# Kernel tuning notes

Measured on AMD Instinct MI355X. Metric: run time of the kernel, lower is better.

Reference implementation:

```python
import jax, jax.numpy as jnp
import numpy as np

B, S, DIM = 4, 4096, 1024
BASE_COUPLING = 0.1
NUM_CYCLES = 3


def _gelu(x):
    # torch nn.GELU default = exact erf formulation
    return jax.nn.gelu(x, approximate=False)


def setup_inputs() -> dict:
    key = jax.random.key(0)
    ks = jax.random.split(key, 9)
    d = DIM

    def w(k, fan_in, fan_out):
        return (jax.random.normal(k, (fan_in, fan_out), dtype=jnp.float32)
                / np.sqrt(fan_in).astype(np.float32))

    inp = {"x": jax.random.normal(ks[0], (B, S, d), dtype=jnp.float32)}
    # coupling_net: dim -> dim -> dim/2 -> dim/4 -> 1
    cn_dims = [(d, d), (d, d // 2), (d // 2, d // 4), (d // 4, 1)]
    for i, (a, b) in enumerate(cn_dims):
        inp[f"cn_w{i+1}"] = w(ks[1 + i], a, b)
        inp[f"cn_b{i+1}"] = jnp.zeros((b,), dtype=jnp.float32)
    # global_context_net: dim -> dim/2 -> dim/4 -> 1
    gc_dims = [(d, d // 2), (d // 2, d // 4), (d // 4, 1)]
    for i, (a, b) in enumerate(gc_dims):
        inp[f"gc_w{i+1}"] = w(ks[5 + i], a, b)
        inp[f"gc_b{i+1}"] = jnp.zeros((b,), dtype=jnp.float32)
    inp["adaptive_range"] = jnp.full((1,), 0.2, dtype=jnp.float32)
    return inp


def _coupling_net(h, w1, b1, w2, b2, w3, b3, w4, b4):
    h = _gelu(h @ w1 + b1)
    h = _gelu(h @ w2 + b2)
    h = _gelu(h @ w3 + b3)
    return jax.nn.sigmoid(h @ w4 + b4)  # [..., 1]


def _global_net(h, w1, b1, w2, b2, w3, b3):
    h = _gelu(h @ w1 + b1)
    h = _gelu(h @ w2 + b2)
    return jax.nn.sigmoid(h @ w3 + b3)  # [b, 1, 1]


def _twist(x):
    # x: [b, s, dim]; omega = first half, pi = second half;
    # each split again into real/imag halves -> quarters [or, oi, pr, pim].
    # omega_new = [pr, -pim], pi_new = [-or, oi]  (position-independent elementwise swap)
    o_r, o_i, p_r, p_i = jnp.split(x, 4, axis=-1)
    return jnp.concatenate([p_r, -p_i, -o_r, o_i], axis=-1)


def reference(x, cn_w1, cn_b1, cn_w2, cn_b2, cn_w3, cn_b3, cn_w4, cn_b4,
              gc_w1, gc_b1, gc_w2, gc_b2, gc_w3, gc_b3, adaptive_range):
    global_context = x.mean(axis=1, keepdims=True)  # [b, 1, dim]
    gf = _global_net(global_context, gc_w1, gc_b1, gc_w2, gc_b2, gc_w3, gc_b3)  # [b,1,1]
    out = x
    for _ in range(NUM_CYCLES):
        tf = _coupling_net(out, cn_w1, cn_b1, cn_w2, cn_b2, cn_w3, cn_b3, cn_w4, cn_b4)  # [b,s,1]
        combined = 0.7 * gf + 0.3 * tf
        coupling = BASE_COUPLING + adaptive_range * (combined - 0.5) * 2.0  # [b,s,1]
        out = out + coupling * _twist(out)
    return out
```

## Files before the change

kernel.cpp:

```cpp
#include <hip/hip_runtime.h>
#include <hip/hip_bf16.h>

#define PB 4
#define PS 4096
#define PD 1024
#define ROWS (PB * PS)
#define NUM_CYCLES 3
#define BASE_COUPLING 0.1f
#define WSCALE 256.0f
#define INV_WSCALE (1.0f / 256.0f)

typedef __attribute__((ext_vector_type(8))) short bf16x8;
typedef __attribute__((ext_vector_type(4))) float f32x4;

__device__ __forceinline__ float geluf(float x) {
    return 0.5f * x * (1.0f + erff(x * 0.70710678118654752440f));
}
__device__ __forceinline__ float gelu_fast(float x) {
    float u = (x + 0.044715f * x * x * x) * 2.3022077f;
    return x * __builtin_amdgcn_rcpf(1.0f + exp2f(-u));
}
__device__ __forceinline__ float sigmf_(float x) {
    return 1.0f / (1.0f + expf(-x));
}
__device__ __forceinline__ uint2 pk4(float4 v) {
    __hip_bfloat16 h[4] = {__float2bfloat16(v.x), __float2bfloat16(v.y),
                           __float2bfloat16(v.z), __float2bfloat16(v.w)};
    return *reinterpret_cast<uint2*>(h);
}
__device__ __forceinline__ float4 axpy4(float4 a, float s, float4 b) {
    return make_float4(fmaf(s, b.x, a.x), fmaf(s, b.y, a.y),
                       fmaf(s, b.z, a.z), fmaf(s, b.w, a.w));
}
__device__ __forceinline__ float bf2f(unsigned short u) {
    unsigned int w = ((unsigned int)u) << 16;
    return __builtin_bit_cast(float, w);
}
__device__ __forceinline__ float4 ubf2f4(uint2 u) {
    unsigned short h[4];
    *reinterpret_cast<uint2*>(h) = u;
    return make_float4(bf2f(h[0]), bf2f(h[1]), bf2f(h[2]), bf2f(h[3]));
}
__device__ __forceinline__ unsigned char f2e4m3(float x) {
    unsigned int u = __builtin_bit_cast(unsigned int, x);
    unsigned int s = (u >> 24) & 0x80u;
    float ax = __builtin_fabsf(x);
    if (!(ax >= 0.015625f)) return (unsigned char)s;
    if (ax >= 464.0f) return (unsigned char)(s | 0x7Eu);
    unsigned int au = u & 0x7FFFFFFFu;
    unsigned int lsb = (au >> 20) & 1u;
    au += 0x0007FFFFu + lsb;
    unsigned int e = (au >> 23) - 127u + 7u;
    unsigned int m = (au >> 20) & 7u;
    if (e >= 16u) return (unsigned char)(s | 0x7Eu);
    return (unsigned char)(s | (e << 3) | m);
}
__device__ __forceinline__ unsigned int pk8(float4 v) {
    return (unsigned int)f2e4m3(v.x) | ((unsigned int)f2e4m3(v.y) << 8) |
           ((unsigned int)f2e4m3(v.z) << 16) | ((unsigned int)f2e4m3(v.w) << 24);
}

#define GLD_LDS16(gsrc, ldst)                                                        \
    __builtin_amdgcn_global_load_lds(                                                \
        (const __attribute__((address_space(1))) void*)(gsrc),                       \
        (__attribute__((address_space(3))) void*)(ldst), 16, 0, 0)

#define ASM_VMCNT4() asm volatile("s_waitcnt vmcnt(4)" ::: "memory")
#define ASM_VMCNT0() asm volatile("s_waitcnt vmcnt(0)" ::: "memory")
#define ASM_LGKM0()  asm volatile("s_waitcnt lgkmcnt(0)" ::: "memory")
#define SCHED_FENCE() __builtin_amdgcn_sched_barrier(0)

__global__ __launch_bounds__(256) void copy_mean_cvt_kernel(const float* __restrict__ x,
                                                            unsigned char* __restrict__ outb8,
                                                            float* __restrict__ part) {
    int b = blockIdx.x >> 7, sc = blockIdx.x & 127;
    size_t base = ((size_t)b * PS + (size_t)sc * 32) * PD;
    const float4* x4 = reinterpret_cast<const float4*>(x + base);
    unsigned int* o8 = reinterpret_cast<unsigned int*>(outb8 + base);
    int t = threadIdx.x;
    float4 acc = make_float4(0.f, 0.f, 0.f, 0.f);
    for (int r = 0; r < 32; ++r) {
        float4 v = x4[r * 256 + t];
        o8[r * 256 + t] = pk8(v);
        acc.x += v.x; acc.y += v.y; acc.z += v.z; acc.w += v.w;
    }
    reinterpret_cast<float4*>(part + ((size_t)(b * 128 + sc)) * PD)[t] = acc;
}

__global__ __launch_bounds__(256) void mean_stage2(const float* __restrict__ part,
                                                   float* __restrict__ gc) {
    int b = blockIdx.x, t = threadIdx.x;
    float4 s = make_float4(0.f, 0.f, 0.f, 0.f);
    for (int c = 0; c < 128; ++c) {
        float4 v = reinterpret_cast<const float4*>(part + ((size_t)(b * 128 + c)) * PD)[t];
        s.x += v.x; s.y += v.y; s.z += v.z; s.w += v.w;
    }
    s.x *= (1.0f / 4096.0f); s.y *= (1.0f / 4096.0f);
    s.z *= (1.0f / 4096.0f); s.w *= (1.0f / 4096.0f);
    reinterpret_cast<float4*>(gc + (size_t)b * PD)[t] = s;
}

__global__ __launch_bounds__(256) void transpose_w_kernel(const float* __restrict__ W,
                                                          __hip_bfloat16* __restrict__ Wt,
                                                          int K, int N) {
    __shared__ float t[32][33];
    int k0 = blockIdx.x * 32, n0 = blockIdx.y * 32;
    int tx = threadIdx.x & 31, ty = threadIdx.x >> 5;
#pragma unroll
    for (int i = 0; i < 32; i += 8)
        t[ty + i][tx] = W[(size_t)(k0 + ty + i) * N + n0 + tx];
    __syncthreads();
#pragma unroll
    for (int i = 0; i < 32; i += 8)
        Wt[(size_t)(n0 + ty + i) * K + k0 + tx] = __float2bfloat16(t[tx][ty + i]);
}

__global__ __launch_bounds__(256) void transpose_w8_kernel(const float* __restrict__ W,
                                                           unsigned char* __restrict__ Wt8,
                                                           int K, int N) {
    __shared__ float t[32][33];
    int k0 = blockIdx.x * 32, n0 = blockIdx.y * 32;
    int tx = threadIdx.x & 31, ty = threadIdx.x >> 5;
#pragma unroll
    for (int i = 0; i < 32; i += 8)
        t[ty + i][tx] = W[(size_t)(k0 + ty + i) * N + n0 + tx];
    __syncthreads();
#pragma unroll
    for (int i = 0; i < 32; i += 8)
        Wt8[(size_t)(n0 + ty + i) * K + k0 + tx] = f2e4m3(t[tx][ty + i] * WSCALE);
}

__global__ __launch_bounds__(256) void gn1_kernel(const float* __restrict__ gc,
                                                  const float* __restrict__ w1,
                                                  const float* __restrict__ b1,
                                                  float* __restrict__ g1) {
    __shared__ float gcs[1024];
    __shared__ float red[4][64];
    int b = blockIdx.x, j0 = blockIdx.y * 64;
    int t = threadIdx.x, wave = t >> 6, lane = t & 63;
    for (int i = t; i < 1024; i += 256) gcs[i] = gc[(size_t)b * PD + i];
    __syncthreads();
    int j = j0 + lane;
    float a = 0.f;
    int k0 = wave * 256;
    for (int k = k0; k < k0 + 256; ++k) a += gcs[k] * w1[(size_t)k * 512 + j];
    red[wave][lane] = a;
    __syncthreads();
    if (wave == 0) {
        float v = red[0][lane] + red[1][lane] + red[2][lane] + red[3][lane] + b1[j];
        g1[(size_t)b * 512 + j] = geluf(v);
    }
}

__global__ __launch_bounds__(256) void gn2_kernel(const float* __restrict__ g1,
                                                  const float* __restrict__ w2,
                                                  const float* __restrict__ b2,
                                                  float* __restrict__ g2) {
    __shared__ float g1s[512];
    __shared__ float red[4][64];
    int b = blockIdx.x, j0 = blockIdx.y * 64;
    int t = threadIdx.x, wave = t >> 6, lane = t & 63;
    for (int i = t; i < 512; i += 256) g1s[i] = g1[(size_t)b * 512 + i];
    __syncthreads();
    int j = j0 + lane;
    float a = 0.f;
    int k0 = wave * 128;
    for (int k = k0; k < k0 + 128; ++k) a += g1s[k] * w2[(size_t)k * 256 + j];
    red[wave][lane] = a;
    __syncthreads();
    if (wave == 0) {
        float v = red[0][lane] + red[1][lane] + red[2][lane] + red[3][lane] + b2[j];
        g2[(size_t)b * 256 + j] = geluf(v);
    }
}

__global__ __launch_bounds__(256) void gn3_kernel(const float* __restrict__ g2,
                                                  const float* __restrict__ w3,
                                                  const float* __restrict__ b3,
                                                  float* __restrict__ gf) {
    __shared__ float red[256];
    int b = blockIdx.x, t = threadIdx.x;
    red[t] = g2[(size_t)b * 256 + t] * w3[t];
    __syncthreads();
    for (int s = 128; s > 0; s >>= 1) {
        if (t < s) red[t] += red[t + s];
        __syncthreads();
    }
    if (t == 0) gf[b] = sigmf_(red[0] + b3[0]);
}

template <int OUTFP8>
__global__ __launch_bounds__(256, 2) void gemm128f8_kernel(
    const unsigned char* __restrict__ A,
    const unsigned char* __restrict__ Wt,
    const float* __restrict__ bias,
    unsigned char* __restrict__ C8,
    __hip_bfloat16* __restrict__ Cb,
    int K, int N) {
    __shared__ __align__(16) unsigned char Als[2][128 * 64];
    __shared__ __align__(16) unsigned char Bls[2][128 * 64];
    const int tid = threadIdx.x;
    const int wave = tid >> 6, lane = tid & 63;
    const int m0 = blockIdx.x * 128, n0 = blockIdx.y * 128;
    const int wr = wave >> 1, wc = wave & 1;
    const int fr = lane & 15, fq = lane >> 4;

    int sr[2], skel[2], sbase[2];
#pragma unroll
    for (int j = 0; j < 2; ++j) {
        int c = j * 256 + tid;
        int row = c >> 2;
        int inner = (c & 3) * 16;
        skel[j] = inner ^ ((row & 6) << 3);
        sr[j] = row;
        sbase[j] = (j * 256 + wave * 64) * 16;
    }
    int aoff[4], boff[4];
#pragma unroll
    for (int f = 0; f < 4; ++f) {
        int rA = wr * 64 + f * 16 + fr;
        aoff[f] = rA * 64 + ((fq * 8) ^ ((rA & 6) << 3));
        int rB = wc * 64 + f * 16 + fr;
        boff[f] = rB * 64 + ((fq * 8) ^ ((rB & 6) << 3));
    }

    f32x4 acc[4][4] = {};
    long av[4], bv[4];

#define STAGE8(bufn, kt) do {                                                         \
    _Pragma("unroll") for (int j = 0; j < 2; ++j) {                                   \
        GLD_LDS16(A + (size_t)(m0 + sr[j]) * K + (kt) + skel[j], (char*)Als[bufn] + sbase[j]); \
        GLD_LDS16(Wt + (size_t)(n0 + sr[j]) * K + (kt) + skel[j], (char*)Bls[bufn] + sbase[j]); \
    }                                                                                 \
} while (0)

    STAGE8(0, 0);
    __syncthreads();

    const int nt = K >> 6;
    for (int t = 0; t < nt; ++t) {
        const int buf = t & 1;
#pragma unroll
        for (int f = 0; f < 4; ++f) bv[f] = *(const long*)(&Bls[buf][boff[f]]);
#pragma unroll
        for (int f = 0; f < 4; ++f) av[f] = *(const long*)(&Als[buf][aoff[f]]);
        if (t + 1 < nt) STAGE8(buf ^ 1, (t + 1) << 6);
        __builtin_amdgcn_s_setprio(1);
#pragma unroll
        for (int mi = 0; mi < 4; ++mi)
#pragma unroll
            for (int ni = 0; ni < 4; ++ni)
                acc[mi][ni] = __builtin_amdgcn_mfma_f32_16x16x32_fp8_fp8(
                    av[mi], bv[ni], acc[mi][ni], 0, 0, 0);
        __builtin_amdgcn_s_setprio(0);
#pragma unroll
        for (int f = 0; f < 4; ++f) bv[f] = *(const long*)(&Bls[buf][boff[f] ^ 32]);
#pragma unroll
        for (int f = 0; f < 4; ++f) av[f] = *(const long*)(&Als[buf][aoff[f] ^ 32]);
        __builtin_amdgcn_s_setprio(1);
#pragma unroll
        for (int mi = 0; mi < 4; ++mi)
#pragma unroll
            for (int ni = 0; ni < 4; ++ni)
                acc[mi][ni] = __builtin_amdgcn_mfma_f32_16x16x32_fp8_fp8(
                    av[mi], bv[ni], acc[mi][ni], 0, 0, 0);
        __builtin_amdgcn_s_setprio(0);
        __syncthreads();
    }

#pragma unroll
    for (int mi = 0; mi < 4; ++mi) {
#pragma unroll
        for (int ni = 0; ni < 4; ++ni) {
            int n = n0 + wc * 64 + ni * 16 + fr;
            float bs = bias[n];
#pragma unroll
            for (int r = 0; r < 4; ++r) {
                int m = m0 + wr * 64 + mi * 16 + fq * 4 + r;
                float v = gelu_fast(fmaf(acc[mi][ni][r], INV_WSCALE, bs));
                if (OUTFP8) C8[(size_t)m * N + n] = f2e4m3(v);
                else        Cb[(size_t)m * N + n] = __float2bfloat16(v);
            }
        }
    }
#undef STAGE8
}

__global__ __launch_bounds__(256, 2) void gemm128b64_pdot_kernel(
    const __hip_bfloat16* __restrict__ A,
    const __hip_bfloat16* __restrict__ Wt,
    const float* __restrict__ bias,
    const float* __restrict__ w4,
    float* __restrict__ pdot,
    int K, int N) {
    __shared__ __align__(16) __hip_bfloat16 Als[2][128 * 64];
    __shared__ __align__(16) __hip_bfloat16 Bls[2][128 * 64];
    __shared__ float spd[128][2];
    const int tid = threadIdx.x;
    const int wave = tid >> 6, lane = tid & 63;
    const int m0 = blockIdx.x * 128, n0 = blockIdx.y * 128;
    const int nb = blockIdx.y;
    const int wr = wave >> 1, wc = wave & 1;
    const int fr = lane & 15, fq = lane >> 4;

    int sr[4], sk[4], sbb[4];
#pragma unroll
    for (int j = 0; j < 4; ++j) {
        int c = wave * 64 + j * 256 + lane;
        int P = c * 16;
        int L = P ^ (((P >> 7) & 7) << 4);
        sr[j] = L >> 7;
        sk[j] = (L & 127) >> 1;
        sbb[j] = (wave * 64 + j * 256) * 16;
    }
    int abyte[4], bbyte[4];
#pragma unroll
    for (int f = 0; f < 4; ++f) {
        int rowA = wr * 64 + f * 16 + fr;
        abyte[f] = (rowA * 128 + fq * 16) ^ ((rowA & 7) << 4);
        int rowB = wc * 64 + f * 16 + fr;
        bbyte[f] = (rowB * 128 + fq * 16) ^ ((rowB & 7) << 4);
    }

    f32x4 acc[4][4] = {};
    bf16x8 av[4][2], bv[4][2];

#define STAGE(bufn, kt) do {                                                         \
    _Pragma("unroll") for (int j = 0; j < 4; ++j) {                                  \
        GLD_LDS16(A + (size_t)(m0 + sr[j]) * K + (kt) + sk[j], (char*)Als[bufn] + sbb[j]); \
        GLD_LDS16(Wt + (size_t)(n0 + sr[j]) * K + (kt) + sk[j], (char*)Bls[bufn] + sbb[j]); \
    }                                                                                \
} while (0)

    STAGE(0, 0);
    __syncthreads();

    const int nt = K >> 6;
    for (int t = 0; t < nt; ++t) {
        const int buf = t & 1;
#pragma unroll
        for (int ni = 0; ni < 4; ++ni)
#pragma unroll
            for (int kk = 0; kk < 2; ++kk)
                bv[ni][kk] = *(const bf16x8*)((const char*)&Bls[buf][0] + (bbyte[ni] ^ (kk << 6)));
#pragma unroll
        for (int mi = 0; mi < 4; ++mi)
#pragma unroll
            for (int kk = 0; kk < 2; ++kk)
                av[mi][kk] = *(const bf16x8*)((const char*)&Als[buf][0] + (abyte[mi] ^ (kk << 6)));
        if (t + 1 < nt) STAGE(buf ^ 1, (t + 1) << 6);
        __builtin_amdgcn_s_setprio(1);
#pragma unroll
        for (int kk = 0; kk < 2; ++kk)
#pragma unroll
            for (int mi = 0; mi < 4; ++mi)
#pragma unroll
                for (int ni = 0; ni < 4; ++ni)
                    acc[mi][ni] = __builtin_amdgcn_mfma_f32_16x16x32_bf16(
                        av[mi][kk], bv[ni][kk], acc[mi][ni], 0, 0, 0);
        __builtin_amdgcn_s_setprio(0);
        __syncthreads();
    }

    float pd[4][4];
#pragma unroll
    for (int mi = 0; mi < 4; ++mi)
#pragma unroll
        for (int r = 0; r < 4; ++r) {
            float s = 0.f;
#pragma unroll
            for (int ni = 0; ni < 4; ++ni) {
                int n = n0 + wc * 64 + ni * 16 + fr;
                s += gelu_fast(acc[mi][ni][r] + bias[n]) * w4[n];
            }
            pd[mi][r] = s;
        }
#pragma unroll
    for (int off = 1; off < 16; off <<= 1)
#pragma unroll
        for (int mi = 0; mi < 4; ++mi)
#pragma unroll
            for (int r = 0; r < 4; ++r)
                pd[mi][r] += __shfl_xor(pd[mi][r], off);
    if (fr == 0) {
#pragma unroll
        for (int mi = 0; mi < 4; ++mi)
#pragma unroll
            for (int r = 0; r < 4; ++r)
                spd[wr * 64 + mi * 16 + fq * 4 + r][wc] = pd[mi][r];
    }
    __syncthreads();
    if (tid < 128) pdot[(size_t)(m0 + tid) * 2 + nb] = spd[tid][0] + spd[tid][1];
#undef STAGE
}

__global__ __launch_bounds__(256) void tf_update_kernel(
    const float* __restrict__ srcf, const __hip_bfloat16* __restrict__ srcb, int use_bf,
    const float* __restrict__ pdot,
    const float* __restrict__ b4,
    const float* __restrict__ gf, const float* __restrict__ arp,
    float* __restrict__ out, __hip_bfloat16* __restrict__ outb,
    unsigned char* __restrict__ outb8, int wf, int wb, int w8) {
    const int wid = threadIdx.x >> 6, lane = threadIdx.x & 63;
    const int r = blockIdx.x * 4 + wid;
    const int b = r >> 12;

    float2 pv = reinterpret_cast<const float2*>(pdot)[r];
    float tf = sigmf_(pv.x + pv.y + b4[0]);
    float comb = 0.7f * gf[b] + 0.3f * tf;
    float c = BASE_COUPLING + arp[0] * (comb - 0.5f) * 2.0f;

    float4 o_r, o_i, p_r, p_i;
    if (use_bf) {
        const uint2* s2 = reinterpret_cast<const uint2*>(srcb + (size_t)r * PD);
        o_r = ubf2f4(s2[lane]);
        o_i = ubf2f4(s2[64 + lane]);
        p_r = ubf2f4(s2[128 + lane]);
        p_i = ubf2f4(s2[192 + lane]);
    } else {
        const float4* s4 = reinterpret_cast<const float4*>(srcf + (size_t)r * PD);
        o_r = s4[lane];
        o_i = s4[64 + lane];
        p_r = s4[128 + lane];
        p_i = s4[192 + lane];
    }
    float4 n0 = axpy4(o_r, c, p_r);
    float4 n1 = axpy4(o_i, -c, p_i);
    float4 n2 = axpy4(p_r, -c, o_r);
    float4 n3 = axpy4(p_i, c, o_i);
    if (wf) {
        float4* row4 = reinterpret_cast<float4*>(out + (size_t)r * PD);
        row4[lane] = n0;
        row4[64 + lane] = n1;
        row4[128 + lane] = n2;
        row4[192 + lane] = n3;
    }
    if (wb) {
        uint2* rb4 = reinterpret_cast<uint2*>(outb + (size_t)r * PD);
        rb4[lane] = pk4(n0);
        rb4[64 + lane] = pk4(n1);
        rb4[128 + lane] = pk4(n2);
        rb4[192 + lane] = pk4(n3);
    }
    if (w8) {
        unsigned int* r8 = reinterpret_cast<unsigned int*>(outb8 + (size_t)r * PD);
        r8[lane] = pk8(n0);
        r8[64 + lane] = pk8(n1);
        r8[128 + lane] = pk8(n2);
        r8[192 + lane] = pk8(n3);
    }
}

extern "C" void kernel_launch(void* const* d_in, const int* in_sizes, int n_in,
                              void* d_out, int out_size, void* d_ws, size_t ws_size,
                              hipStream_t stream) {
    const float* x     = (const float*)d_in[0];
    const float* cn_w1 = (const float*)d_in[1];
    const float* cn_b1 = (const float*)d_in[2];
    const float* cn_w2 = (const float*)d_in[3];
    const float* cn_b2 = (const float*)d_in[4];
    const float* cn_w3 = (const float*)d_in[5];
    const float* cn_b3 = (const float*)d_in[6];
    const float* cn_w4 = (const float*)d_in[7];
    const float* cn_b4 = (const float*)d_in[8];
    const float* gc_w1 = (const float*)d_in[9];
    const float* gc_b1 = (const float*)d_in[10];
    const float* gc_w2 = (const float*)d_in[11];
    const float* gc_b2 = (const float*)d_in[12];
    const float* gc_w3 = (const float*)d_in[13];
    const float* gc_b3 = (const float*)d_in[14];
    const float* ar    = (const float*)d_in[15];

    float* out = (float*)d_out;

    char* ws = (char*)d_ws;
    unsigned char* h1_8   = (unsigned char*)(ws);
    __hip_bfloat16* h2    = (__hip_bfloat16*)(ws + ((size_t)16 << 20));
    __hip_bfloat16* outb  = (__hip_bfloat16*)(ws + ((size_t)32 << 20));
    unsigned char* outb8  = (unsigned char*)(ws + ((size_t)64 << 20));
    unsigned char* wt1_8  = (unsigned char*)(ws + ((size_t)80 << 20));
    unsigned char* wt2_8  = (unsigned char*)(ws + ((size_t)81 << 20));
    __hip_bfloat16* wt3   = (__hip_bfloat16*)(ws + ((size_t)81 << 20) + ((size_t)1 << 19));
    float* pdot           = (float*)(ws + ((size_t)82 << 20));
    float* part           = (float*)(ws + ((size_t)83 << 20));
    float* gc             = (float*)(ws + ((size_t)85 << 20));
    float* g1             = gc + 4 * PD;
    float* g2             = g1 + 4 * 512;
    float* gf             = g2 + 4 * 256;

    transpose_w8_kernel<<<dim3(32, 32), 256, 0, stream>>>(cn_w1, wt1_8, 1024, 1024);
    transpose_w8_kernel<<<dim3(32, 16), 256, 0, stream>>>(cn_w2, wt2_8, 1024, 512);
    transpose_w_kernel<<<dim3(16, 8), 256, 0, stream>>>(cn_w3, wt3, 512, 256);

    copy_mean_cvt_kernel<<<512, 256, 0, stream>>>(x, outb8, part);
    mean_stage2<<<PB, 256, 0, stream>>>(part, gc);

    gn1_kernel<<<dim3(PB, 8), 256, 0, stream>>>(gc, gc_w1, gc_b1, g1);
    gn2_kernel<<<dim3(PB, 4), 256, 0, stream>>>(g1, gc_w2, gc_b2, g2);
    gn3_kernel<<<PB, 256, 0, stream>>>(g2, gc_w3, gc_b3, gf);

    for (int cyc = 0; cyc < NUM_CYCLES; ++cyc) {
        gemm128f8_kernel<1><<<dim3(128, 8), 256, 0, stream>>>(
            outb8, wt1_8, cn_b1, h1_8, nullptr, 1024, 1024);
        gemm128f8_kernel<0><<<dim3(128, 4), 256, 0, stream>>>(
            h1_8, wt2_8, cn_b2, nullptr, h2, 1024, 512);
        gemm128b64_pdot_kernel<<<dim3(128, 2), 256, 0, stream>>>(
            h2, wt3, cn_b3, cn_w4, pdot, 512, 256);
        int last = (cyc + 1 == NUM_CYCLES);
        tf_update_kernel<<<ROWS / 4, 256, 0, stream>>>(
            x, outb, (cyc > 0) ? 1 : 0, pdot, cn_b4, gf, ar,
            out, outb, outb8, last ? 1 : 0, last ? 0 : 1, last ? 0 : 1);
    }
}
```

Before: 319.3 us.

## Move third coupling GEMM to FP8 and use 32x32 MFMA for first GEMM

The second GEMM now writes FP8 activations instead of bf16, and the third GEMM (with the fused w4 dot) switches from bf16 to FP8 MFMA with scaled FP8 weights. This halves the h2 traffic and doubles the MFMA rate for that layer. A new first-layer GEMM variant uses 32x32x16 FP8 MFMA tiles, which need fewer LDS fragment reads per FLOP. The cost is extra quantization error from FP8 on h2 and W3, and a different register and epilogue layout in the first GEMM.

```diff
diff --git a/kernel.cpp b/kernel.cpp
--- a/kernel.cpp
+++ b/kernel.cpp
@@ -12,6 +12,7 @@
 
 typedef __attribute__((ext_vector_type(8))) short bf16x8;
 typedef __attribute__((ext_vector_type(4))) float f32x4;
+typedef __attribute__((ext_vector_type(16))) float f32x16;
 
 __device__ __forceinline__ float geluf(float x) {
     return 0.5f * x * (1.0f + erff(x * 0.70710678118654752440f));
@@ -65,11 +66,6 @@
         (const __attribute__((address_space(1))) void*)(gsrc),                       \
         (__attribute__((address_space(3))) void*)(ldst), 16, 0, 0)
 
-#define ASM_VMCNT4() asm volatile("s_waitcnt vmcnt(4)" ::: "memory")
-#define ASM_VMCNT0() asm volatile("s_waitcnt vmcnt(0)" ::: "memory")
-#define ASM_LGKM0()  asm volatile("s_waitcnt lgkmcnt(0)" ::: "memory")
-#define SCHED_FENCE() __builtin_amdgcn_sched_barrier(0)
-
 __global__ __launch_bounds__(256) void copy_mean_cvt_kernel(const float* __restrict__ x,
                                                             unsigned char* __restrict__ outb8,
                                                             float* __restrict__ part) {
@@ -100,21 +96,6 @@
     reinterpret_cast<float4*>(gc + (size_t)b * PD)[t] = s;
 }
 
-__global__ __launch_bounds__(256) void transpose_w_kernel(const float* __restrict__ W,
-                                                          __hip_bfloat16* __restrict__ Wt,
-                                                          int K, int N) {
-    __shared__ float t[32][33];
-    int k0 = blockIdx.x * 32, n0 = blockIdx.y * 32;
-    int tx = threadIdx.x & 31, ty = threadIdx.x >> 5;
-#pragma unroll
-    for (int i = 0; i < 32; i += 8)
-        t[ty + i][tx] = W[(size_t)(k0 + ty + i) * N + n0 + tx];
-    __syncthreads();
-#pragma unroll
-    for (int i = 0; i < 32; i += 8)
-        Wt[(size_t)(n0 + ty + i) * K + k0 + tx] = __float2bfloat16(t[tx][ty + i]);
-}
-
 __global__ __launch_bounds__(256) void transpose_w8_kernel(const float* __restrict__ W,
                                                            unsigned char* __restrict__ Wt8,
                                                            int K, int N) {
@@ -187,6 +168,109 @@
         __syncthreads();
     }
     if (t == 0) gf[b] = sigmf_(red[0] + b3[0]);
+}
+
+template <int OUTFP8>
+__global__ __launch_bounds__(256, 2) void gemm128f8x32_kernel(
+    const unsigned char* __restrict__ A,
+    const unsigned char* __restrict__ Wt,
+    const float* __restrict__ bias,
+    unsigned char* __restrict__ C8,
+    __hip_bfloat16* __restrict__ Cb,
+    int K, int N) {
+    __shared__ __align__(16) unsigned char Als[2][128 * 64];
+    __shared__ __align__(16) unsigned char Bls[2][128 * 64];
+    const int tid = threadIdx.x;
+    const int wave = tid >> 6, lane = tid & 63;
+    const int m0 = blockIdx.x * 128, n0 = blockIdx.y * 128;
+    const int wr = wave >> 1, wc = wave & 1;
+    const int l31 = lane & 31, fq2 = lane >> 5;
+
+    int sr[2], skel[2], sbase[2];
+#pragma unroll
+    for (int j = 0; j < 2; ++j) {
+        int c = j * 256 + tid;
+        int row = c >> 2;
+        int inner = (c & 3) * 16;
+        skel[j] = inner ^ ((row & 6) << 3);
+        sr[j] = row;
+        sbase[j] = (j * 256 + wave * 64) * 16;
+    }
+    int aoff[2][4], boff[2][4];
+#pragma unroll
+    for (int rb = 0; rb < 2; ++rb)
+#pragma unroll
+        for (int ks = 0; ks < 4; ++ks) {
+            int rowA = wr * 64 + rb * 32 + l31;
+            aoff[rb][ks] = rowA * 64 + ((ks * 16) ^ ((rowA & 6) << 3)) + fq2 * 8;
+            int rowB = wc * 64 + rb * 32 + l31;
+            boff[rb][ks] = rowB * 64 + ((ks * 16) ^ ((rowB & 6) << 3)) + fq2 * 8;
+        }
+
+    f32x16 acc[2][2] = {};
+    long av[4], bv[2][4];
+
+#define STAGE8(bufn, kt) do {                                                         \
+    _Pragma("unroll") for (int j = 0; j < 2; ++j) {                                   \
+        GLD_LDS16(A + (size_t)(m0 + sr[j]) * K + (kt) + skel[j], (char*)Als[bufn] + sbase[j]); \
+        GLD_LDS16(Wt + (size_t)(n0 + sr[j]) * K + (kt) + skel[j], (char*)Bls[bufn] + sbase[j]); \
+    }                                                                                 \
+} while (0)
+
+    STAGE8(0, 0);
+    __syncthreads();
+
+    const int nt = K >> 6;
+    for (int t = 0; t < nt; ++t) {
+        const int buf = t & 1;
+#pragma unroll
+        for (int rb = 0; rb < 2; ++rb)
+#pragma unroll
+            for (int ks = 0; ks < 4; ++ks)
+                bv[rb][ks] = *(const long*)(&Bls[buf][boff[rb][ks]]);
+#pragma unroll
+        for (int ks = 0; ks < 4; ++ks)
+            av[ks] = *(const long*)(&Als[buf][aoff[0][ks]]);
+        if (t + 1 < nt) STAGE8(buf ^ 1, (t + 1) << 6);
+        __builtin_amdgcn_s_setprio(1);
+#pragma unroll
+        for (int ks = 0; ks < 4; ++ks)
+#pragma unroll
+            for (int tj = 0; tj < 2; ++tj)
+                acc[0][tj] = __builtin_amdgcn_mfma_f32_32x32x16_fp8_fp8(
+                    av[ks], bv[tj][ks], acc[0][tj], 0, 0, 0);
+        __builtin_amdgcn_s_setprio(0);
+#pragma unroll
+        for (int ks = 0; ks < 4; ++ks)
+            av[ks] = *(const long*)(&Als[buf][aoff[1][ks]]);
+        __builtin_amdgcn_s_setprio(1);
+#pragma unroll
+        for (int ks = 0; ks < 4; ++ks)
+#pragma unroll
+            for (int tj = 0; tj < 2; ++tj)
+                acc[1][tj] = __builtin_amdgcn_mfma_f32_32x32x16_fp8_fp8(
+                    av[ks], bv[tj][ks], acc[1][tj], 0, 0, 0);
+        __builtin_amdgcn_s_setprio(0);
+        __syncthreads();
+    }
+
+#pragma unroll
+    for (int ti = 0; ti < 2; ++ti) {
+#pragma unroll
+        for (int tj = 0; tj < 2; ++tj) {
+            int n = n0 + wc * 64 + tj * 32 + l31;
+            float bs = bias[n];
+#pragma unroll
+            for (int reg = 0; reg < 16; ++reg) {
+                int row = (reg & 3) + 8 * (reg >> 2) + 4 * fq2;
+                int m = m0 + wr * 64 + ti * 32 + row;
+                float v = gelu_fast(fmaf(acc[ti][tj][reg], INV_WSCALE, bs));
+                if (OUTFP8) C8[(size_t)m * N + n] = f2e4m3(v);
+                else        Cb[(size_t)m * N + n] = __float2bfloat16(v);
+            }
+        }
+    }
+#undef STAGE8
 }
 
 template <int OUTFP8>
@@ -286,15 +370,15 @@
 #undef STAGE8
 }
 
-__global__ __launch_bounds__(256, 2) void gemm128b64_pdot_kernel(
-    const __hip_bfloat16* __restrict__ A,
-    const __hip_bfloat16* __restrict__ Wt,
+__global__ __launch_bounds__(256, 2) void gemm128f8_pdot_kernel(
+    const unsigned char* __restrict__ A,
+    const unsigned char* __restrict__ Wt,
     const float* __restrict__ bias,
     const float* __restrict__ w4,
     float* __restrict__ pdot,
     int K, int N) {
-    __shared__ __align__(16) __hip_bfloat16 Als[2][128 * 64];
-    __shared__ __align__(16) __hip_bfloat16 Bls[2][128 * 64];
+    __shared__ __align__(16) unsigned char Als[2][128 * 64];
+    __shared__ __align__(16) unsigned char Bls[2][128 * 64];
     __shared__ float spd[128][2];
     const int tid = threadIdx.x;
     const int wave = tid >> 6, lane = tid & 63;
@@ -303,61 +387,65 @@
     const int wr = wave >> 1, wc = wave & 1;
     const int fr = lane & 15, fq = lane >> 4;
 
-    int sr[4], sk[4], sbb[4];
-#pragma unroll
-    for (int j = 0; j < 4; ++j) {
-        int c = wave * 64 + j * 256 + lane;
-        int P = c * 16;
-        int L = P ^ (((P >> 7) & 7) << 4);
-        sr[j] = L >> 7;
-        sk[j] = (L & 127) >> 1;
-        sbb[j] = (wave * 64 + j * 256) * 16;
-    }
-    int abyte[4], bbyte[4];
+    int sr[2], skel[2], sbase[2];
+#pragma unroll
+    for (int j = 0; j < 2; ++j) {
+        int c = j * 256 + tid;
+        int row = c >> 2;
+        int inner = (c & 3) * 16;
+        skel[j] = inner ^ ((row & 6) << 3);
+        sr[j] = row;
+        sbase[j] = (j * 256 + wave * 64) * 16;
+    }
+    int aoff[4], boff[4];
 #pragma unroll
     for (int f = 0; f < 4; ++f) {
-        int rowA = wr * 64 + f * 16 + fr;
-        abyte[f] = (rowA * 128 + fq * 16) ^ ((rowA & 7) << 4);
-        int rowB = wc * 64 + f * 16 + fr;
-        bbyte[f] = (rowB * 128 + fq * 16) ^ ((rowB & 7) << 4);
+        int rA = wr * 64 + f * 16 + fr;
+        aoff[f] = rA * 64 + ((fq * 8) ^ ((rA & 6) << 3));
+        int rB = wc * 64 + f * 16 + fr;
+        boff[f] = rB * 64 + ((fq * 8) ^ ((rB & 6) << 3));
     }
 
     f32x4 acc[4][4] = {};
-    bf16x8 av[4][2], bv[4][2];
-
-#define STAGE(bufn, kt) do {                                                         \
-    _Pragma("unroll") for (int j = 0; j < 4; ++j) {                                  \
-        GLD_LDS16(A + (size_t)(m0 + sr[j]) * K + (kt) + sk[j], (char*)Als[bufn] + sbb[j]); \
-        GLD_LDS16(Wt + (size_t)(n0 + sr[j]) * K + (kt) + sk[j], (char*)Bls[bufn] + sbb[j]); \
-    }                                                                                \
+    long av[4], bv[4];
+
+#define STAGE8(bufn, kt) do {                                                         \
+    _Pragma("unroll") for (int j = 0; j < 2; ++j) {                                   \
+        GLD_LDS16(A + (size_t)(m0 + sr[j]) * K + (kt) + skel[j], (char*)Als[bufn] + sbase[j]); \
+        GLD_LDS16(Wt + (size_t)(n0 + sr[j]) * K + (kt) + skel[j], (char*)Bls[bufn] + sbase[j]); \
+    }                                                                                 \
 } while (0)
 
-    STAGE(0, 0);
+    STAGE8(0, 0);
     __syncthreads();
 
     const int nt = K >> 6;
     for (int t = 0; t < nt; ++t) {
         const int buf = t & 1;
 #pragma unroll
-        for (int ni = 0; ni < 4; ++ni)
-#pragma unroll
-            for (int kk = 0; kk < 2; ++kk)
-                bv[ni][kk] = *(const bf16x8*)((const char*)&Bls[buf][0] + (bbyte[ni] ^ (kk << 6)));
+        for (int f = 0; f < 4; ++f) bv[f] = *(const long*)(&Bls[buf][boff[f]]);
+#pragma unroll
+        for (int f = 0; f < 4; ++f) av[f] = *(const long*)(&Als[buf][aoff[f]]);
+        if (t + 1 < nt) STAGE8(buf ^ 1, (t + 1) << 6);
+        __builtin_amdgcn_s_setprio(1);
 #pragma unroll
         for (int mi = 0; mi < 4; ++mi)
 #pragma unroll
-            for (int kk = 0; kk < 2; ++kk)
-                av[mi][kk] = *(const bf16x8*)((const char*)&Als[buf][0] + (abyte[mi] ^ (kk << 6)));
-        if (t + 1 < nt) STAGE(buf ^ 1, (t + 1) << 6);
+            for (int ni = 0; ni < 4; ++ni)
+                acc[mi][ni] = __builtin_amdgcn_mfma_f32_16x16x32_fp8_fp8(
+                    av[mi], bv[ni], acc[mi][ni], 0, 0, 0);
+        __builtin_amdgcn_s_setprio(0);
+#pragma unroll
+        for (int f = 0; f < 4; ++f) bv[f] = *(const long*)(&Bls[buf][boff[f] ^ 32]);
+#pragma unroll
+        for (int f = 0; f < 4; ++f) av[f] = *(const long*)(&Als[buf][aoff[f] ^ 32]);
         __builtin_amdgcn_s_setprio(1);
 #pragma unroll
-        for (int kk = 0; kk < 2; ++kk)
-#pragma unroll
-            for (int mi = 0; mi < 4; ++mi)
-#pragma unroll
-                for (int ni = 0; ni < 4; ++ni)
-                    acc[mi][ni] = __builtin_amdgcn_mfma_f32_16x16x32_bf16(
-                        av[mi][kk], bv[ni][kk], acc[mi][ni], 0, 0, 0);
+        for (int mi = 0; mi < 4; ++mi)
+#pragma unroll
+            for (int ni = 0; ni < 4; ++ni)
+                acc[mi][ni] = __builtin_amdgcn_mfma_f32_16x16x32_fp8_fp8(
+                    av[mi], bv[ni], acc[mi][ni], 0, 0, 0);
         __builtin_amdgcn_s_setprio(0);
         __syncthreads();
     }
@@ -371,7 +459,7 @@
 #pragma unroll
             for (int ni = 0; ni < 4; ++ni) {
                 int n = n0 + wc * 64 + ni * 16 + fr;
-                s += gelu_fast(acc[mi][ni][r] + bias[n]) * w4[n];
+                s += gelu_fast(fmaf(acc[mi][ni][r], INV_WSCALE, bias[n])) * w4[n];
             }
             pd[mi][r] = s;
         }
@@ -391,7 +479,7 @@
     }
     __syncthreads();
     if (tid < 128) pdot[(size_t)(m0 + tid) * 2 + nb] = spd[tid][0] + spd[tid][1];
-#undef STAGE
+#undef STAGE8
 }
 
 __global__ __launch_bounds__(256) void tf_update_kernel(
@@ -475,22 +563,22 @@
 
     char* ws = (char*)d_ws;
     unsigned char* h1_8   = (unsigned char*)(ws);
-    __hip_bfloat16* h2    = (__hip_bfloat16*)(ws + ((size_t)16 << 20));
-    __hip_bfloat16* outb  = (__hip_bfloat16*)(ws + ((size_t)32 << 20));
-    unsigned char* outb8  = (unsigned char*)(ws + ((size_t)64 << 20));
-    unsigned char* wt1_8  = (unsigned char*)(ws + ((size_t)80 << 20));
-    unsigned char* wt2_8  = (unsigned char*)(ws + ((size_t)81 << 20));
-    __hip_bfloat16* wt3   = (__hip_bfloat16*)(ws + ((size_t)81 << 20) + ((size_t)1 << 19));
-    float* pdot           = (float*)(ws + ((size_t)82 << 20));
-    float* part           = (float*)(ws + ((size_t)83 << 20));
-    float* gc             = (float*)(ws + ((size_t)85 << 20));
+    unsigned char* h2_8   = (unsigned char*)(ws + ((size_t)16 << 20));
+    __hip_bfloat16* outb  = (__hip_bfloat16*)(ws + ((size_t)24 << 20));
+    unsigned char* outb8  = (unsigned char*)(ws + ((size_t)56 << 20));
+    unsigned char* wt1_8  = (unsigned char*)(ws + ((size_t)72 << 20));
+    unsigned char* wt2_8  = (unsigned char*)(ws + ((size_t)73 << 20));
+    unsigned char* wt3_8  = (unsigned char*)(ws + ((size_t)73 << 20) + ((size_t)1 << 19));
+    float* pdot           = (float*)(ws + ((size_t)74 << 20));
+    float* part           = (float*)(ws + ((size_t)75 << 20));
+    float* gc             = (float*)(ws + ((size_t)77 << 20));
     float* g1             = gc + 4 * PD;
     float* g2             = g1 + 4 * 512;
     float* gf             = g2 + 4 * 256;
 
     transpose_w8_kernel<<<dim3(32, 32), 256, 0, stream>>>(cn_w1, wt1_8, 1024, 1024);
     transpose_w8_kernel<<<dim3(32, 16), 256, 0, stream>>>(cn_w2, wt2_8, 1024, 512);
-    transpose_w_kernel<<<dim3(16, 8), 256, 0, stream>>>(cn_w3, wt3, 512, 256);
+    transpose_w8_kernel<<<dim3(16, 8), 256, 0, stream>>>(cn_w3, wt3_8, 512, 256);
 
     copy_mean_cvt_kernel<<<512, 256, 0, stream>>>(x, outb8, part);
     mean_stage2<<<PB, 256, 0, stream>>>(part, gc);
@@ -500,12 +588,12 @@
     gn3_kernel<<<PB, 256, 0, stream>>>(g2, gc_w3, gc_b3, gf);
 
     for (int cyc = 0; cyc < NUM_CYCLES; ++cyc) {
-        gemm128f8_kernel<1><<<dim3(128, 8), 256, 0, stream>>>(
+        gemm128f8x32_kernel<1><<<dim3(128, 8), 256, 0, stream>>>(
             outb8, wt1_8, cn_b1, h1_8, nullptr, 1024, 1024);
-        gemm128f8_kernel<0><<<dim3(128, 4), 256, 0, stream>>>(
-            h1_8, wt2_8, cn_b2, nullptr, h2, 1024, 512);
-        gemm128b64_pdot_kernel<<<dim3(128, 2), 256, 0, stream>>>(
-            h2, wt3, cn_b3, cn_w4, pdot, 512, 256);
+        gemm128f8_kernel<1><<<dim3(128, 4), 256, 0, stream>>>(
+            h1_8, wt2_8, cn_b2, h2_8, nullptr, 1024, 512);
+        gemm128f8_pdot_kernel<<<dim3(128, 2), 256, 0, stream>>>(
+            h2_8, wt3_8, cn_b3, cn_w4, pdot, 512, 256);
         int last = (cyc + 1 == NUM_CYCLES);
         tf_update_kernel<<<ROWS / 4, 256, 0, stream>>>(
             x, outb, (cyc > 0) ? 1 : 0, pdot, cn_b4, gf, ar,
```

Result: slower. 347.5 us (+8.8%).
